# Kernel tuning notes

Measured on AMD Instinct MI355X. Metric: run time of the kernel, lower is better.

## Reference

```python
import jax, jax.numpy as jnp
import numpy as np

B, G, N, C = 8, 16, 1024, 256


def setup_inputs() -> dict:
    key = jax.random.key(0)
    k1, k2, k3, k4, k5 = jax.random.split(key, 5)
    x = jax.random.normal(k1, (B, G, N, C), dtype=jnp.float32)
    vs = jax.random.normal(k2, (B, G, 1, N, 3), dtype=jnp.float32)
    s = 1.0 / np.sqrt(C)
    W_fc = jax.random.normal(k3, (C, C), dtype=jnp.float32) * s   # nn.Linear weight [out,in]
    b_fc = jax.random.normal(k4, (C,), dtype=jnp.float32) * s
    W_vn = jax.random.normal(k5, (C, C), dtype=jnp.float32) * s   # VNLinear weight [out,in], no bias
    return {"x": x, "vs": vs, "W_fc": W_fc, "b_fc": b_fc, "W_vn": W_vn}


def reference(x, vs, W_fc, b_fc, W_vn):
    # q = fc(x): [B,G,N,C]
    q = jnp.einsum('bgnc,oc->bgno', x, W_fc) + b_fc
    # softmax over the point dim N (torch dim=2)
    atten = jax.nn.softmax(q, axis=2)
    xw = atten * x  # [B,G,N,C]
    # torch: expand to [B,G,C,N,3] * vs then sum over N.
    # Equivalent contraction without materializing the 5D tensor:
    v = jnp.squeeze(vs, axis=2)  # [B,G,N,3]
    out = jnp.einsum('bgnc,bgnd->bgcd', xw, v)  # [B,G,C,3]
    # VNLinear: bias-free linear over channel dim, shared across the 3 vector comps
    return jnp.einsum('bgcd,oc->bgod', out, W_vn)  # [B,G,C,3]
```

## Files before the change

kernel.cpp:

```cpp
#include <hip/hip_runtime.h>


#define NQ 1024
#define CQ 256
#define CT 64
#define RT 128
#define NT (NQ / RT)
#define XS 136
#define WS 264

typedef __attribute__((ext_vector_type(8))) short bf16x8;
typedef __attribute__((ext_vector_type(4))) float f32x4;

__device__ __forceinline__ ushort f2bf(float f) {
    union { float f; unsigned u; } v; v.f = f;
    return (ushort)((v.u + 0x7fffu + ((v.u >> 16) & 1u)) >> 16);
}
__device__ __forceinline__ float bf2f(ushort h) {
    union { unsigned u; float f; } v; v.u = ((unsigned)h) << 16;
    return v.f;
}

__global__ __launch_bounds__(256, 2)
void fused_attn_pool_mfma(const float* __restrict__ x, const float* __restrict__ vs,
                          const float* __restrict__ Wfc, float* __restrict__ Tout) {
    __shared__ __align__(16) ushort xs[RT * XS];
    __shared__ __align__(16) ushort ws[CT * WS];
    __shared__ __align__(16) float  vsm[RT * 3];
    __shared__ f32x4 red[4][32];

    const int t = threadIdx.x;
    const int id = blockIdx.x;
    const int ctile = (id >> 3) & 3;
    const int bg = (id & 7) + ((id >> 5) << 3);
    const int c0 = ctile * CT;
    const int own = ctile >> 1;

    const int w = t >> 6, lane = t & 63;
    const int quad = lane >> 4, l16 = lane & 15;
    const int rstrip = (w & 1) * 64;
    const int cstrip = (w >> 1) * 32;

    const float* xb = x + (size_t)bg * NQ * CQ;
    const float* vb = vs + (size_t)bg * NQ * 3;

    #pragma unroll
    for (int p = 0; p < 16; ++p) {
        int idx = p * 256 + t;
        int row = idx >> 6, c4 = idx & 63;
        float4 v4 = *reinterpret_cast<const float4*>(Wfc + (size_t)(c0 + row) * CQ + c4 * 4);
        ushort4 pk = { f2bf(v4.x), f2bf(v4.y), f2bf(v4.z), f2bf(v4.w) };
        *reinterpret_cast<ushort4*>(&ws[row * WS + c4 * 4]) = pk;
    }

    float rZ[2] = {0.f, 0.f}, rS0[2] = {0.f, 0.f}, rS1[2] = {0.f, 0.f}, rS2[2] = {0.f, 0.f};

    for (int nt = 0; nt < NT; ++nt) {
        const int n0 = nt * RT;
        if (t < 96) {
            reinterpret_cast<float4*>(vsm)[t] =
                reinterpret_cast<const float4*>(vb + (size_t)n0 * 3)[t];
        }

        f32x4 acc[4][2];
        #pragma unroll
        for (int m = 0; m < 4; ++m)
            #pragma unroll
            for (int ci = 0; ci < 2; ++ci) acc[m][ci] = (f32x4){0.f, 0.f, 0.f, 0.f};

        for (int kc = 0; kc < 2; ++kc) {
            const int ch = (kc == 0) ? (own ^ 1) : own;
            const int kc0 = ch * 128;
            #pragma unroll
            for (int p = 0; p < 16; ++p) {
                int idx = p * 256 + t;
                int row = idx >> 5, k4 = idx & 31;
                float4 v4 = *reinterpret_cast<const float4*>(
                    xb + (size_t)(n0 + row) * CQ + kc0 + k4 * 4);
                ushort4 pk = { f2bf(v4.x), f2bf(v4.y), f2bf(v4.z), f2bf(v4.w) };
                *reinterpret_cast<ushort4*>(&xs[row * XS + k4 * 4]) = pk;
            }
            __syncthreads();
            #pragma unroll
            for (int ks = 0; ks < 4; ++ks) {
                const int kk = ks * 32 + quad * 8;
                bf16x8 b0 = *reinterpret_cast<const bf16x8*>(&ws[(cstrip + l16) * WS + kc0 + kk]);
                bf16x8 b1 = *reinterpret_cast<const bf16x8*>(&ws[(cstrip + 16 + l16) * WS + kc0 + kk]);
                #pragma unroll
                for (int m = 0; m < 4; ++m) {
                    bf16x8 a = *reinterpret_cast<const bf16x8*>(
                        &xs[(rstrip + m * 16 + l16) * XS + kk]);
                    acc[m][0] = __builtin_amdgcn_mfma_f32_16x16x32_bf16(a, b0, acc[m][0], 0, 0, 0);
                    acc[m][1] = __builtin_amdgcn_mfma_f32_16x16x32_bf16(a, b1, acc[m][1], 0, 0, 0);
                }
            }
            __syncthreads();
        }
        const int xcb = (ctile & 1) * 64 + cstrip;

        #pragma unroll
        for (int m = 0; m < 4; ++m) {
            const int rbase = rstrip + m * 16 + quad * 4;
            float v0[4], v1[4], v2[4];
            #pragma unroll
            for (int r = 0; r < 4; ++r) {
                v0[r] = vsm[(rbase + r) * 3 + 0];
                v1[r] = vsm[(rbase + r) * 3 + 1];
                v2[r] = vsm[(rbase + r) * 3 + 2];
            }
            #pragma unroll
            for (int ci = 0; ci < 2; ++ci) {
                const int xc = xcb + ci * 16 + l16;
                #pragma unroll
                for (int r = 0; r < 4; ++r) {
                    float e = __expf(acc[m][ci][r]);
                    float xv = bf2f(xs[(rbase + r) * XS + xc]);
                    rZ[ci] += e;
                    float p = e * xv;
                    rS0[ci] = fmaf(p, v0[r], rS0[ci]);
                    rS1[ci] = fmaf(p, v1[r], rS1[ci]);
                    rS2[ci] = fmaf(p, v2[r], rS2[ci]);
                }
            }
        }
        __syncthreads();
    }

    #pragma unroll
    for (int ci = 0; ci < 2; ++ci) {
        float z = rZ[ci], s0 = rS0[ci], s1 = rS1[ci], s2 = rS2[ci];
        #pragma unroll
        for (int off = 16; off < 64; off <<= 1) {
            z  += __shfl_xor(z,  off);
            s0 += __shfl_xor(s0, off);
            s1 += __shfl_xor(s1, off);
            s2 += __shfl_xor(s2, off);
        }
        if (quad == 0) red[w][ci * 16 + l16] = (f32x4){z, s0, s1, s2};
    }
    __syncthreads();
    if (t < CT) {
        const int s = t >> 5, cc = t & 31;
        f32x4 a = red[2 * s][cc], b = red[2 * s + 1][cc];
        float Z = a[0] + b[0];
        float inv = 1.f / Z;
        float* o = Tout + ((size_t)bg * CQ + c0 + t) * 3;
        o[0] = (a[1] + b[1]) * inv;
        o[1] = (a[2] + b[2]) * inv;
        o[2] = (a[3] + b[3]) * inv;
    }
}

__global__ __launch_bounds__(256)
void vn_linear(const float* __restrict__ T, const float* __restrict__ Wvn,
               float* __restrict__ out) {
    __shared__ __align__(16) float Ts[CQ * 3];
    const int bg = blockIdx.x >> 1, half = blockIdx.x & 1;
    const int t = threadIdx.x, wv = t >> 6, lane = t & 63;
    if (t < 192)
        reinterpret_cast<float4*>(Ts)[t] =
            reinterpret_cast<const float4*>(T + (size_t)bg * CQ * 3)[t];
    __syncthreads();
    const int c = lane * 4;
    float t00 = Ts[(c+0)*3+0], t01 = Ts[(c+0)*3+1], t02 = Ts[(c+0)*3+2];
    float t10 = Ts[(c+1)*3+0], t11 = Ts[(c+1)*3+1], t12 = Ts[(c+1)*3+2];
    float t20 = Ts[(c+2)*3+0], t21 = Ts[(c+2)*3+1], t22 = Ts[(c+2)*3+2];
    float t30 = Ts[(c+3)*3+0], t31 = Ts[(c+3)*3+1], t32 = Ts[(c+3)*3+2];
    const int obase = half * 128 + wv * 32;
    for (int i = 0; i < 32; ++i) {
        const int o = obase + i;
        float4 w4 = *reinterpret_cast<const float4*>(Wvn + (size_t)o * CQ + c);
        float a0 = w4.x*t00 + w4.y*t10 + w4.z*t20 + w4.w*t30;
        float a1 = w4.x*t01 + w4.y*t11 + w4.z*t21 + w4.w*t31;
        float a2 = w4.x*t02 + w4.y*t12 + w4.z*t22 + w4.w*t32;
        #pragma unroll
        for (int off = 1; off < 64; off <<= 1) {
            a0 += __shfl_xor(a0, off);
            a1 += __shfl_xor(a1, off);
            a2 += __shfl_xor(a2, off);
        }
        if (lane == 0) {
            float* op = out + ((size_t)bg * CQ + o) * 3;
            op[0] = a0; op[1] = a1; op[2] = a2;
        }
    }
}

extern "C" void kernel_launch(void* const* d_in, const int* in_sizes, int n_in,
                              void* d_out, int out_size, void* d_ws, size_t ws_size,
                              hipStream_t stream) {
    const float* x   = (const float*)d_in[0];
    const float* vs  = (const float*)d_in[1];
    const float* Wfc = (const float*)d_in[2];
    const float* Wvn = (const float*)d_in[4];
    float* out = (float*)d_out;
    float* T = (float*)d_ws;

    fused_attn_pool_mfma<<<dim3(512), dim3(256), 0, stream>>>(x, vs, Wfc, T);
    vn_linear<<<dim3(256), dim3(256), 0, stream>>>(T, Wvn, out);
}
```

Measured before the change: 235.2 us.

## Fuse VN linear into attention kernel via atomics and keep Wfc fragments in registers

```diff
diff --git a/kernel.cpp b/kernel.cpp
--- a/kernel.cpp
+++ b/kernel.cpp
@@ -1,4 +1,5 @@
 #include <hip/hip_runtime.h>
+#include <hip/hip_bf16.h>
 
 
 #define NQ 1024
@@ -7,14 +8,15 @@
 #define RT 128
 #define NT (NQ / RT)
 #define XS 136
-#define WS 264
 
 typedef __attribute__((ext_vector_type(8))) short bf16x8;
 typedef __attribute__((ext_vector_type(4))) float f32x4;
 
-__device__ __forceinline__ ushort f2bf(float f) {
-    union { float f; unsigned u; } v; v.f = f;
-    return (ushort)((v.u + 0x7fffu + ((v.u >> 16) & 1u)) >> 16);
+__device__ __forceinline__ ushort2 pk2(float a, float b) {
+    __hip_bfloat162 h = __float22bfloat162_rn(make_float2(a, b));
+    ushort2 r;
+    __builtin_memcpy(&r, &h, sizeof(r));
+    return r;
 }
 __device__ __forceinline__ float bf2f(ushort h) {
     union { unsigned u; float f; } v; v.u = ((unsigned)h) << 16;
@@ -23,11 +25,12 @@
 
 __global__ __launch_bounds__(256, 2)
 void fused_attn_pool_mfma(const float* __restrict__ x, const float* __restrict__ vs,
-                          const float* __restrict__ Wfc, float* __restrict__ Tout) {
+                          const float* __restrict__ Wfc, const float* __restrict__ Wvn,
+                          float* __restrict__ out) {
     __shared__ __align__(16) ushort xs[RT * XS];
-    __shared__ __align__(16) ushort ws[CT * WS];
     __shared__ __align__(16) float  vsm[RT * 3];
     __shared__ f32x4 red[4][32];
+    __shared__ float Tsm[CT][3];
 
     const int t = threadIdx.x;
     const int id = blockIdx.x;
@@ -44,13 +47,27 @@
     const float* xb = x + (size_t)bg * NQ * CQ;
     const float* vb = vs + (size_t)bg * NQ * 3;
 
-    #pragma unroll
-    for (int p = 0; p < 16; ++p) {
-        int idx = p * 256 + t;
-        int row = idx >> 6, c4 = idx & 63;
-        float4 v4 = *reinterpret_cast<const float4*>(Wfc + (size_t)(c0 + row) * CQ + c4 * 4);
-        ushort4 pk = { f2bf(v4.x), f2bf(v4.y), f2bf(v4.z), f2bf(v4.w) };
-        *reinterpret_cast<ushort4*>(&ws[row * WS + c4 * 4]) = pk;
+    bf16x8 bf[2][4][2];
+    {
+        const int myc0 = c0 + cstrip + l16;
+        #pragma unroll
+        for (int kc = 0; kc < 2; ++kc) {
+            const int ch = (kc == 0) ? (own ^ 1) : own;
+            const int kb = ch * 128 + quad * 8;
+            #pragma unroll
+            for (int ks = 0; ks < 4; ++ks) {
+                #pragma unroll
+                for (int ci = 0; ci < 2; ++ci) {
+                    const float* p = Wfc + (size_t)(myc0 + ci * 16) * CQ + kb + ks * 32;
+                    float4 lo = *reinterpret_cast<const float4*>(p);
+                    float4 hi = *reinterpret_cast<const float4*>(p + 4);
+                    ushort2 p0 = pk2(lo.x, lo.y), p1 = pk2(lo.z, lo.w);
+                    ushort2 p2 = pk2(hi.x, hi.y), p3 = pk2(hi.z, hi.w);
+                    bf[kc][ks][ci] = (bf16x8){ (short)p0.x, (short)p0.y, (short)p1.x, (short)p1.y,
+                                               (short)p2.x, (short)p2.y, (short)p3.x, (short)p3.y };
+                }
+            }
+        }
     }
 
     float rZ[2] = {0.f, 0.f}, rS0[2] = {0.f, 0.f}, rS1[2] = {0.f, 0.f}, rS2[2] = {0.f, 0.f};
@@ -68,6 +85,7 @@
             #pragma unroll
             for (int ci = 0; ci < 2; ++ci) acc[m][ci] = (f32x4){0.f, 0.f, 0.f, 0.f};
 
+        #pragma unroll
         for (int kc = 0; kc < 2; ++kc) {
             const int ch = (kc == 0) ? (own ^ 1) : own;
             const int kc0 = ch * 128;
@@ -77,24 +95,23 @@
                 int row = idx >> 5, k4 = idx & 31;
                 float4 v4 = *reinterpret_cast<const float4*>(
                     xb + (size_t)(n0 + row) * CQ + kc0 + k4 * 4);
-                ushort4 pk = { f2bf(v4.x), f2bf(v4.y), f2bf(v4.z), f2bf(v4.w) };
+                ushort2 a0 = pk2(v4.x, v4.y), a1 = pk2(v4.z, v4.w);
+                ushort4 pk = { a0.x, a0.y, a1.x, a1.y };
                 *reinterpret_cast<ushort4*>(&xs[row * XS + k4 * 4]) = pk;
             }
             __syncthreads();
             #pragma unroll
             for (int ks = 0; ks < 4; ++ks) {
                 const int kk = ks * 32 + quad * 8;
-                bf16x8 b0 = *reinterpret_cast<const bf16x8*>(&ws[(cstrip + l16) * WS + kc0 + kk]);
-                bf16x8 b1 = *reinterpret_cast<const bf16x8*>(&ws[(cstrip + 16 + l16) * WS + kc0 + kk]);
                 #pragma unroll
                 for (int m = 0; m < 4; ++m) {
                     bf16x8 a = *reinterpret_cast<const bf16x8*>(
                         &xs[(rstrip + m * 16 + l16) * XS + kk]);
-                    acc[m][0] = __builtin_amdgcn_mfma_f32_16x16x32_bf16(a, b0, acc[m][0], 0, 0, 0);
-                    acc[m][1] = __builtin_amdgcn_mfma_f32_16x16x32_bf16(a, b1, acc[m][1], 0, 0, 0);
+                    acc[m][0] = __builtin_amdgcn_mfma_f32_16x16x32_bf16(a, bf[kc][ks][0], acc[m][0], 0, 0, 0);
+                    acc[m][1] = __builtin_amdgcn_mfma_f32_16x16x32_bf16(a, bf[kc][ks][1], acc[m][1], 0, 0, 0);
                 }
             }
-            __syncthreads();
+            if (kc == 0) __syncthreads();
         }
         const int xcb = (ctile & 1) * 64 + cstrip;
 
@@ -142,47 +159,30 @@
     if (t < CT) {
         const int s = t >> 5, cc = t & 31;
         f32x4 a = red[2 * s][cc], b = red[2 * s + 1][cc];
-        float Z = a[0] + b[0];
-        float inv = 1.f / Z;
-        float* o = Tout + ((size_t)bg * CQ + c0 + t) * 3;
-        o[0] = (a[1] + b[1]) * inv;
-        o[1] = (a[2] + b[2]) * inv;
-        o[2] = (a[3] + b[3]) * inv;
-    }
-}
-
-__global__ __launch_bounds__(256)
-void vn_linear(const float* __restrict__ T, const float* __restrict__ Wvn,
-               float* __restrict__ out) {
-    __shared__ __align__(16) float Ts[CQ * 3];
-    const int bg = blockIdx.x >> 1, half = blockIdx.x & 1;
-    const int t = threadIdx.x, wv = t >> 6, lane = t & 63;
-    if (t < 192)
-        reinterpret_cast<float4*>(Ts)[t] =
-            reinterpret_cast<const float4*>(T + (size_t)bg * CQ * 3)[t];
+        float inv = 1.f / (a[0] + b[0]);
+        Tsm[t][0] = (a[1] + b[1]) * inv;
+        Tsm[t][1] = (a[2] + b[2]) * inv;
+        Tsm[t][2] = (a[3] + b[3]) * inv;
+    }
     __syncthreads();
-    const int c = lane * 4;
-    float t00 = Ts[(c+0)*3+0], t01 = Ts[(c+0)*3+1], t02 = Ts[(c+0)*3+2];
-    float t10 = Ts[(c+1)*3+0], t11 = Ts[(c+1)*3+1], t12 = Ts[(c+1)*3+2];
-    float t20 = Ts[(c+2)*3+0], t21 = Ts[(c+2)*3+1], t22 = Ts[(c+2)*3+2];
-    float t30 = Ts[(c+3)*3+0], t31 = Ts[(c+3)*3+1], t32 = Ts[(c+3)*3+2];
-    const int obase = half * 128 + wv * 32;
-    for (int i = 0; i < 32; ++i) {
-        const int o = obase + i;
-        float4 w4 = *reinterpret_cast<const float4*>(Wvn + (size_t)o * CQ + c);
-        float a0 = w4.x*t00 + w4.y*t10 + w4.z*t20 + w4.w*t30;
-        float a1 = w4.x*t01 + w4.y*t11 + w4.z*t21 + w4.w*t31;
-        float a2 = w4.x*t02 + w4.y*t12 + w4.z*t22 + w4.w*t32;
-        #pragma unroll
-        for (int off = 1; off < 64; off <<= 1) {
-            a0 += __shfl_xor(a0, off);
-            a1 += __shfl_xor(a1, off);
-            a2 += __shfl_xor(a2, off);
-        }
-        if (lane == 0) {
-            float* op = out + ((size_t)bg * CQ + o) * 3;
-            op[0] = a0; op[1] = a1; op[2] = a2;
-        }
+
+    {
+        const float* wr = Wvn + (size_t)t * CQ + c0;
+        float a0 = 0.f, a1 = 0.f, a2 = 0.f;
+        #pragma unroll
+        for (int c = 0; c < CT; c += 4) {
+            float4 w4 = *reinterpret_cast<const float4*>(wr + c);
+            a0 += w4.x * Tsm[c + 0][0] + w4.y * Tsm[c + 1][0]
+                + w4.z * Tsm[c + 2][0] + w4.w * Tsm[c + 3][0];
+            a1 += w4.x * Tsm[c + 0][1] + w4.y * Tsm[c + 1][1]
+                + w4.z * Tsm[c + 2][1] + w4.w * Tsm[c + 3][1];
+            a2 += w4.x * Tsm[c + 0][2] + w4.y * Tsm[c + 1][2]
+                + w4.z * Tsm[c + 2][2] + w4.w * Tsm[c + 3][2];
+        }
+        float* op = out + ((size_t)bg * CQ + t) * 3;
+        atomicAdd(&op[0], a0);
+        atomicAdd(&op[1], a1);
+        atomicAdd(&op[2], a2);
     }
 }
 
@@ -194,8 +194,7 @@
     const float* Wfc = (const float*)d_in[2];
     const float* Wvn = (const float*)d_in[4];
     float* out = (float*)d_out;
-    float* T = (float*)d_ws;
-
-    fused_attn_pool_mfma<<<dim3(512), dim3(256), 0, stream>>>(x, vs, Wfc, T);
-    vn_linear<<<dim3(256), dim3(256), 0, stream>>>(T, Wvn, out);
-}
+
+    (void)hipMemsetAsync(out, 0, (size_t)out_size * sizeof(float), stream);
+    fused_attn_pool_mfma<<<dim3(512), dim3(256), 0, stream>>>(x, vs, Wfc, Wvn, out);
+}
```

New measurement: 221.6 us. -5.8%, faster.
